# Optimization experiments

Hardware: AMD Instinct MI355X
Metric: run time of the kernel (lower is better)

Reference implementation:

```python
import jax, jax.numpy as jnp
import numpy as np

N, E, F, D = 50000, 800000, 128, 32
CUTOFF = 5.0


def swish(x):
    return x * jax.nn.sigmoid(x)


def setup_inputs() -> dict:
    key = jax.random.key(0)
    ks = jax.random.split(key, 15)
    sF = 1.0 / np.sqrt(F)
    inp = {
        "x": jax.random.normal(ks[0], (N, F), jnp.float32),
        # distances in [0, 6) so some edges lie beyond the 5.0 cutoff
        "rij": jax.random.uniform(ks[1], (E,), jnp.float32) * 6.0,
        "vij": jax.random.normal(ks[2], (E, 3), jnp.float32),
        "src": jax.random.randint(ks[3], (E,), 0, N),
        "dst": jax.random.randint(ks[4], (E,), 0, N),
        # transform: Dense(F,F,swish) -> Dense(F,D,swish)
        "W1": jax.random.normal(ks[5], (F, F), jnp.float32) * sF,
        "b1": jnp.zeros((F,), jnp.float32),
        "W2": jax.random.normal(ks[6], (F, D), jnp.float32) * sF,
        "b2": jnp.zeros((D,), jnp.float32),
        # transform2 (cross_product branch)
        "W1b": jax.random.normal(ks[7], (F, F), jnp.float32) * sF,
        "b1b": jnp.zeros((F,), jnp.float32),
        "W2b": jax.random.normal(ks[8], (F, D), jnp.float32) * sF,
        "b2b": jnp.zeros((D,), jnp.float32),
        # mix: Dense(3, 1), no activation
        "w_mix": jax.random.normal(ks[9], (3,), jnp.float32) * (1.0 / np.sqrt(3.0)),
        "b_mix": jnp.zeros((1,), jnp.float32),
    }
    return inp


def reference(x, rij, vij, src, dst, W1, b1, W2, b2, W1b, b1b, W2b, b2b, w_mix, b_mix):
    # node transforms: q, q2 in [N, D]
    q = swish(swish(x @ W1 + b1) @ W2 + b2)
    q2 = swish(swish(x @ W1b + b1b) @ W2b + b2b)

    # cosine cutoff on per-edge distance [E]
    c = 0.5 * (jnp.cos(jnp.pi * rij / CUTOFF) + 1.0)
    c = c * (rij < CUTOFF).astype(c.dtype)

    # e_mul_u: edge vij [E,1,3] * source-node q [E,D,1] -> [E,D,3], then cutoff scale
    mu_ij = vij[:, None, :] * q[src][:, :, None] * c[:, None, None]
    mu = jax.ops.segment_sum(mu_ij, dst, num_segments=N)  # [N,D,3]

    mu_ij2 = vij[:, None, :] * q2[src][:, :, None] * c[:, None, None]
    mu2 = jax.ops.segment_sum(mu_ij2, dst, num_segments=N)  # [N,D,3]

    mu3 = jnp.cross(mu, mu2, axis=-1)  # [N,D,3]
    stacked = jnp.stack([mu, mu2, mu3], axis=-1)  # [N,D,3,3]
    out = stacked @ w_mix + b_mix[0]  # mix Dense(3,1), squeezed -> [N,D,3]
    return out
```

## Files before the change

### kernel.cpp

```cpp
#include <hip/hip_runtime.h>
#include <hip/hip_bf16.h>

#define N_NODES 50000
#define E_EDGES 800000
#define F_DIM 128
#define D_DIM 32
#define CUTOFF 5.0f
#define PI_F 3.14159265358979f
#define SCAN_BLOCKS ((N_NODES + 255) / 256)

#define MLP_BLOCKS ((N_NODES + 31) / 32)
#define HIST_BLOCKS ((E_EDGES + 255) / 256)
#define XPAD 132

__device__ __forceinline__ float swishf(float x) { return x / (1.0f + expf(-x)); }

__global__ __launch_bounds__(256, 4)
void mlp_hist(const float* __restrict__ x,
              const float* __restrict__ W1a, const float* __restrict__ b1a,
              const float* __restrict__ W2a, const float* __restrict__ b2a,
              const float* __restrict__ W1b, const float* __restrict__ b1b,
              const float* __restrict__ W2b, const float* __restrict__ b2b,
              float* __restrict__ qq,
              const float* __restrict__ rij, const int* __restrict__ dst,
              int* __restrict__ deg) {
  if (blockIdx.x >= MLP_BLOCKS) {
    const int e = (blockIdx.x - MLP_BLOCKS) * 256 + threadIdx.x;
    if (e < E_EDGES && rij[e] < CUTOFF) atomicAdd(&deg[dst[e]], 1);
    return;
  }

  __shared__ float sX[64 * XPAD];

  const int rb = blockIdx.x * 32;
  const int t  = threadIdx.x;
  const int c  = t & 31;
  const int r0 = (t >> 5) * 4;

  {
    const int row = t >> 3;
    const int kq  = t & 7;
    const int rowG = min(rb + row, N_NODES - 1);
    const float* xp = x + (size_t)rowG * F_DIM;
#pragma unroll
    for (int p = 0; p < 4; ++p) {
      const int k0 = kq * 4 + p * 32;
      *(float4*)&sX[row * XPAD + k0] = *(const float4*)&xp[k0];
    }
  }
  __syncthreads();

  float accA[4][4], accB[4][4];
  {
    const float4 ba = *(const float4*)&b1a[4 * c];
    const float4 bb = *(const float4*)&b1b[4 * c];
#pragma unroll
    for (int r = 0; r < 4; ++r) {
      accA[r][0] = ba.x; accA[r][1] = ba.y; accA[r][2] = ba.z; accA[r][3] = ba.w;
      accB[r][0] = bb.x; accB[r][1] = bb.y; accB[r][2] = bb.z; accB[r][3] = bb.w;
    }
  }
  {
    const float* xrow = sX + r0 * XPAD;
    const float* wa_base = W1a + 4 * c;
    const float* wb_base = W1b + 4 * c;
#pragma unroll 2
    for (int k4 = 0; k4 < 32; ++k4) {
      float4 wa[4], wb[4];
#pragma unroll
      for (int kk = 0; kk < 4; ++kk) {
        const size_t off = (size_t)(k4 * 4 + kk) * F_DIM;
        wa[kk] = *(const float4*)(wa_base + off);
        wb[kk] = *(const float4*)(wb_base + off);
      }
      float4 xv[4];
#pragma unroll
      for (int r = 0; r < 4; ++r)
        xv[r] = *(const float4*)&xrow[r * XPAD + k4 * 4];
#pragma unroll
      for (int kk = 0; kk < 4; ++kk) {
#pragma unroll
        for (int r = 0; r < 4; ++r) {
          const float xs = (kk == 0) ? xv[r].x : (kk == 1) ? xv[r].y
                         : (kk == 2) ? xv[r].z : xv[r].w;
          accA[r][0] = fmaf(xs, wa[kk].x, accA[r][0]);
          accA[r][1] = fmaf(xs, wa[kk].y, accA[r][1]);
          accA[r][2] = fmaf(xs, wa[kk].z, accA[r][2]);
          accA[r][3] = fmaf(xs, wa[kk].w, accA[r][3]);
          accB[r][0] = fmaf(xs, wb[kk].x, accB[r][0]);
          accB[r][1] = fmaf(xs, wb[kk].y, accB[r][1]);
          accB[r][2] = fmaf(xs, wb[kk].z, accB[r][2]);
          accB[r][3] = fmaf(xs, wb[kk].w, accB[r][3]);
        }
      }
    }
  }

  __syncthreads();
#pragma unroll
  for (int r = 0; r < 4; ++r) {
    *(float4*)&sX[(r0 + r) * XPAD + 4 * c] =
        make_float4(swishf(accA[r][0]), swishf(accA[r][1]),
                    swishf(accA[r][2]), swishf(accA[r][3]));
    *(float4*)&sX[(32 + r0 + r) * XPAD + 4 * c] =
        make_float4(swishf(accB[r][0]), swishf(accB[r][1]),
                    swishf(accB[r][2]), swishf(accB[r][3]));
  }
  __syncthreads();

  float a2A[4], a2B[4];
  {
    const float bA = b2a[c];
    const float bB = b2b[c];
#pragma unroll
    for (int r = 0; r < 4; ++r) { a2A[r] = bA; a2B[r] = bB; }
  }
  {
    const float* hrowA = sX + r0 * XPAD;
    const float* hrowB = sX + (32 + r0) * XPAD;
#pragma unroll 2
    for (int k4 = 0; k4 < 32; ++k4) {
      float wA[4], wB[4];
#pragma unroll
      for (int kk = 0; kk < 4; ++kk) {
        wA[kk] = W2a[(size_t)(k4 * 4 + kk) * D_DIM + c];
        wB[kk] = W2b[(size_t)(k4 * 4 + kk) * D_DIM + c];
      }
      float4 hA[4], hB[4];
#pragma unroll
      for (int r = 0; r < 4; ++r) {
        hA[r] = *(const float4*)&hrowA[r * XPAD + k4 * 4];
        hB[r] = *(const float4*)&hrowB[r * XPAD + k4 * 4];
      }
#pragma unroll
      for (int kk = 0; kk < 4; ++kk) {
#pragma unroll
        for (int r = 0; r < 4; ++r) {
          const float hsA = (kk == 0) ? hA[r].x : (kk == 1) ? hA[r].y
                          : (kk == 2) ? hA[r].z : hA[r].w;
          const float hsB = (kk == 0) ? hB[r].x : (kk == 1) ? hB[r].y
                          : (kk == 2) ? hB[r].z : hB[r].w;
          a2A[r] = fmaf(hsA, wA[kk], a2A[r]);
          a2B[r] = fmaf(hsB, wB[kk], a2B[r]);
        }
      }
    }
  }

#pragma unroll
  for (int r = 0; r < 4; ++r) {
    const int row = rb + r0 + r;
    if (row < N_NODES) {
      *(float2*)&qq[(size_t)row * 64 + 2 * c] =
          make_float2(swishf(a2A[r]), swishf(a2B[r]));
    }
  }
}

__global__ __launch_bounds__(256)
void scan_blocksum(const int* __restrict__ deg, int* __restrict__ part) {
  __shared__ int red[256];
  const int t = threadIdx.x;
  const int i = blockIdx.x * 256 + t;
  red[t] = (i < N_NODES) ? deg[i] : 0;
  __syncthreads();
#pragma unroll
  for (int off = 128; off > 0; off >>= 1) {
    if (t < off) red[t] += red[t + off];
    __syncthreads();
  }
  if (t == 0) part[blockIdx.x] = red[0];
}

__global__ __launch_bounds__(256)
void scan_partials(int* __restrict__ part, int* __restrict__ row_start) {
  __shared__ int s[256];
  const int t = threadIdx.x;
  const int v = (t < SCAN_BLOCKS) ? part[t] : 0;
  s[t] = v;
  __syncthreads();
  for (int off = 1; off < 256; off <<= 1) {
    const int u = (t >= off) ? s[t - off] : 0;
    __syncthreads();
    s[t] += u;
    __syncthreads();
  }
  if (t < SCAN_BLOCKS) part[t] = s[t] - v;
  if (t == 255) row_start[N_NODES] = s[255];
}

__global__ __launch_bounds__(256)
void scan_write(const int* __restrict__ deg, const int* __restrict__ part,
                int* __restrict__ row_start, int* __restrict__ cursor) {
  __shared__ int s[256];
  const int t = threadIdx.x;
  const int i = blockIdx.x * 256 + t;
  const int v = (i < N_NODES) ? deg[i] : 0;
  s[t] = v;
  __syncthreads();
  for (int off = 1; off < 256; off <<= 1) {
    const int u = (t >= off) ? s[t - off] : 0;
    __syncthreads();
    s[t] += u;
    __syncthreads();
  }
  const int excl = s[t] - v + part[blockIdx.x];
  if (i < N_NODES) { row_start[i] = excl; cursor[i] = excl; }
}

__global__ __launch_bounds__(256)
void edge_reorder(const float* __restrict__ rij, const float* __restrict__ vij,
                  const int* __restrict__ src, const int* __restrict__ dst,
                  int* __restrict__ cursor, float4* __restrict__ recs) {
  const int e = blockIdx.x * 256 + threadIdx.x;
  if (e >= E_EDGES) return;
  const float r = rij[e];
  if (r >= CUTOFF) return;
  const float c = 0.5f * (cosf(r * (PI_F / CUTOFF)) + 1.0f);
  const int pos = atomicAdd(&cursor[dst[e]], 1);
  recs[pos] = make_float4(c * vij[3 * e + 0], c * vij[3 * e + 1],
                          c * vij[3 * e + 2], __int_as_float(src[e]));
}

__global__ __launch_bounds__(256)
void gather_out(const int* __restrict__ row_start, const float4* __restrict__ recs,
                const float2* __restrict__ qq,
                const float* __restrict__ w_mix, const float* __restrict__ b_mix,
                float* __restrict__ out) {
  const int tid = blockIdx.x * 256 + threadIdx.x;
  const int n = tid >> 5;
  const int d = tid & 31;
  if (n >= N_NODES) return;

  const int s0 = row_start[n];
  const int s1 = row_start[n + 1];

  float ax = 0.f, ay = 0.f, az = 0.f, bx = 0.f, by = 0.f, bz = 0.f;
  for (int i = s0; i < s1; i += 4) {
    const int i1 = min(i + 1, s1 - 1);
    const int i2 = min(i + 2, s1 - 1);
    const int i3 = min(i + 3, s1 - 1);
    float4 rc0 = recs[i];
    float4 rc1 = recs[i1];
    float4 rc2 = recs[i2];
    float4 rc3 = recs[i3];
    float2 p0 = qq[__float_as_int(rc0.w) * 32 + d];
    float2 p1 = qq[__float_as_int(rc1.w) * 32 + d];
    float2 p2 = qq[__float_as_int(rc2.w) * 32 + d];
    float2 p3 = qq[__float_as_int(rc3.w) * 32 + d];
    const float m1 = (i + 1 < s1) ? 1.f : 0.f;
    const float m2 = (i + 2 < s1) ? 1.f : 0.f;
    const float m3 = (i + 3 < s1) ? 1.f : 0.f;
    p1.x *= m1; p1.y *= m1;
    p2.x *= m2; p2.y *= m2;
    p3.x *= m3; p3.y *= m3;

    ax += rc0.x * p0.x + rc1.x * p1.x + rc2.x * p2.x + rc3.x * p3.x;
    ay += rc0.y * p0.x + rc1.y * p1.x + rc2.y * p2.x + rc3.y * p3.x;
    az += rc0.z * p0.x + rc1.z * p1.x + rc2.z * p2.x + rc3.z * p3.x;
    bx += rc0.x * p0.y + rc1.x * p1.y + rc2.x * p2.y + rc3.x * p3.y;
    by += rc0.y * p0.y + rc1.y * p1.y + rc2.y * p2.y + rc3.y * p3.y;
    bz += rc0.z * p0.y + rc1.z * p1.y + rc2.z * p2.y + rc3.z * p3.y;
  }

  const float cx = ay * bz - az * by;
  const float cy = az * bx - ax * bz;
  const float cz = ax * by - ay * bx;

  const float w0 = w_mix[0], w1 = w_mix[1], w2 = w_mix[2];
  const float bm = b_mix[0];

  const size_t base = (size_t)tid * 3;
  out[base + 0] = ax * w0 + bx * w1 + cx * w2 + bm;
  out[base + 1] = ay * w0 + by * w1 + cy * w2 + bm;
  out[base + 2] = az * w0 + bz * w1 + cz * w2 + bm;
}

extern "C" void kernel_launch(void* const* d_in, const int* in_sizes, int n_in,
                              void* d_out, int out_size, void* d_ws, size_t ws_size,
                              hipStream_t stream) {
  const float* x     = (const float*)d_in[0];
  const float* rij   = (const float*)d_in[1];
  const float* vij   = (const float*)d_in[2];
  const int*   src   = (const int*)  d_in[3];
  const int*   dst   = (const int*)  d_in[4];
  const float* W1    = (const float*)d_in[5];
  const float* b1    = (const float*)d_in[6];
  const float* W2    = (const float*)d_in[7];
  const float* b2    = (const float*)d_in[8];
  const float* W1b   = (const float*)d_in[9];
  const float* b1b   = (const float*)d_in[10];
  const float* W2b   = (const float*)d_in[11];
  const float* b2b   = (const float*)d_in[12];
  const float* w_mix = (const float*)d_in[13];
  const float* b_mix = (const float*)d_in[14];
  float* out = (float*)d_out;

  float4* recs   = (float4*)d_ws;
  float* qq      = (float*)(recs + E_EDGES);
  int* deg       = (int*)(qq + (size_t)N_NODES * 64);
  int* cursor    = deg + N_NODES;
  int* row_start = cursor + N_NODES;
  int* part      = row_start + N_NODES + 1;

  hipMemsetAsync(deg, 0, sizeof(int) * N_NODES, stream);

  mlp_hist<<<MLP_BLOCKS + HIST_BLOCKS, 256, 0, stream>>>(
      x, W1, b1, W2, b2, W1b, b1b, W2b, b2b, qq, rij, dst, deg);

  scan_blocksum<<<SCAN_BLOCKS, 256, 0, stream>>>(deg, part);
  scan_partials<<<1, 256, 0, stream>>>(part, row_start);
  scan_write<<<SCAN_BLOCKS, 256, 0, stream>>>(deg, part, row_start, cursor);

  const int eb = (E_EDGES + 255) / 256;
  edge_reorder<<<eb, 256, 0, stream>>>(rij, vij, src, dst, cursor, recs);

  gather_out<<<(N_NODES * D_DIM) / 256, 256, 0, stream>>>(
      row_start, recs, (const float2*)qq, w_mix, b_mix, out);
}
```

Measured before the change: 279.8 us.

## Split node MLP across histogram and reorder kernels to overlap edge passes

The node MLP blocks are split into two groups. The first 512 blocks run alongside the degree-histogram pass, and the remaining blocks are fused into the edge-reorder kernel. Edge blocks now come first in each grid, so the atomic-bound edge work overlaps with compute-bound MLP work in both launches. The MLP part is factored into a device function. The 512 split ratio is a tuning choice, and the edge kernel now carries the MLP's launch bounds and shared memory, which may reduce its occupancy.

```diff
diff --git a/kernel.cpp b/kernel.cpp
--- a/kernel.cpp
+++ b/kernel.cpp
@@ -10,29 +10,24 @@
 #define SCAN_BLOCKS ((N_NODES + 255) / 256)
 
 #define MLP_BLOCKS ((N_NODES + 31) / 32)
-#define HIST_BLOCKS ((E_EDGES + 255) / 256)
+#define MLP_PART1 512
+#define MLP_PART2 (MLP_BLOCKS - MLP_PART1)
+#define EDGE_BLOCKS ((E_EDGES + 255) / 256)
 #define XPAD 132
 
 __device__ __forceinline__ float swishf(float x) { return x / (1.0f + expf(-x)); }
 
-__global__ __launch_bounds__(256, 4)
-void mlp_hist(const float* __restrict__ x,
-              const float* __restrict__ W1a, const float* __restrict__ b1a,
-              const float* __restrict__ W2a, const float* __restrict__ b2a,
-              const float* __restrict__ W1b, const float* __restrict__ b1b,
-              const float* __restrict__ W2b, const float* __restrict__ b2b,
-              float* __restrict__ qq,
-              const float* __restrict__ rij, const int* __restrict__ dst,
-              int* __restrict__ deg) {
-  if (blockIdx.x >= MLP_BLOCKS) {
-    const int e = (blockIdx.x - MLP_BLOCKS) * 256 + threadIdx.x;
-    if (e < E_EDGES && rij[e] < CUTOFF) atomicAdd(&deg[dst[e]], 1);
-    return;
-  }
-
+__device__ __forceinline__ void mlp_body(
+    int mb,
+    const float* __restrict__ x,
+    const float* __restrict__ W1a, const float* __restrict__ b1a,
+    const float* __restrict__ W2a, const float* __restrict__ b2a,
+    const float* __restrict__ W1b, const float* __restrict__ b1b,
+    const float* __restrict__ W2b, const float* __restrict__ b2b,
+    float* __restrict__ qq) {
   __shared__ float sX[64 * XPAD];
 
-  const int rb = blockIdx.x * 32;
+  const int rb = mb * 32;
   const int t  = threadIdx.x;
   const int c  = t & 31;
   const int r0 = (t >> 5) * 4;
@@ -157,6 +152,48 @@
   }
 }
 
+__global__ __launch_bounds__(256, 4)
+void hist_mlp1(const float* __restrict__ x,
+               const float* __restrict__ W1a, const float* __restrict__ b1a,
+               const float* __restrict__ W2a, const float* __restrict__ b2a,
+               const float* __restrict__ W1b, const float* __restrict__ b1b,
+               const float* __restrict__ W2b, const float* __restrict__ b2b,
+               float* __restrict__ qq,
+               const float* __restrict__ rij, const int* __restrict__ dst,
+               int* __restrict__ deg) {
+  if (blockIdx.x < EDGE_BLOCKS) {
+    const int e = blockIdx.x * 256 + threadIdx.x;
+    if (e < E_EDGES && rij[e] < CUTOFF) atomicAdd(&deg[dst[e]], 1);
+    return;
+  }
+  mlp_body(blockIdx.x - EDGE_BLOCKS, x, W1a, b1a, W2a, b2a, W1b, b1b, W2b, b2b, qq);
+}
+
+__global__ __launch_bounds__(256, 4)
+void reorder_mlp2(const float* __restrict__ x,
+                  const float* __restrict__ W1a, const float* __restrict__ b1a,
+                  const float* __restrict__ W2a, const float* __restrict__ b2a,
+                  const float* __restrict__ W1b, const float* __restrict__ b1b,
+                  const float* __restrict__ W2b, const float* __restrict__ b2b,
+                  float* __restrict__ qq,
+                  const float* __restrict__ rij, const float* __restrict__ vij,
+                  const int* __restrict__ src, const int* __restrict__ dst,
+                  int* __restrict__ cursor, float4* __restrict__ recs) {
+  if (blockIdx.x < EDGE_BLOCKS) {
+    const int e = blockIdx.x * 256 + threadIdx.x;
+    if (e >= E_EDGES) return;
+    const float r = rij[e];
+    if (r >= CUTOFF) return;
+    const float c = 0.5f * (cosf(r * (PI_F / CUTOFF)) + 1.0f);
+    const int pos = atomicAdd(&cursor[dst[e]], 1);
+    recs[pos] = make_float4(c * vij[3 * e + 0], c * vij[3 * e + 1],
+                            c * vij[3 * e + 2], __int_as_float(src[e]));
+    return;
+  }
+  mlp_body(MLP_PART1 + (blockIdx.x - EDGE_BLOCKS),
+           x, W1a, b1a, W2a, b2a, W1b, b1b, W2b, b2b, qq);
+}
+
 __global__ __launch_bounds__(256)
 void scan_blocksum(const int* __restrict__ deg, int* __restrict__ part) {
   __shared__ int red[256];
@@ -206,20 +243,6 @@
   }
   const int excl = s[t] - v + part[blockIdx.x];
   if (i < N_NODES) { row_start[i] = excl; cursor[i] = excl; }
-}
-
-__global__ __launch_bounds__(256)
-void edge_reorder(const float* __restrict__ rij, const float* __restrict__ vij,
-                  const int* __restrict__ src, const int* __restrict__ dst,
-                  int* __restrict__ cursor, float4* __restrict__ recs) {
-  const int e = blockIdx.x * 256 + threadIdx.x;
-  if (e >= E_EDGES) return;
-  const float r = rij[e];
-  if (r >= CUTOFF) return;
-  const float c = 0.5f * (cosf(r * (PI_F / CUTOFF)) + 1.0f);
-  const int pos = atomicAdd(&cursor[dst[e]], 1);
-  recs[pos] = make_float4(c * vij[3 * e + 0], c * vij[3 * e + 1],
-                          c * vij[3 * e + 2], __int_as_float(src[e]));
 }
 
 __global__ __launch_bounds__(256)
@@ -305,15 +328,16 @@
 
   hipMemsetAsync(deg, 0, sizeof(int) * N_NODES, stream);
 
-  mlp_hist<<<MLP_BLOCKS + HIST_BLOCKS, 256, 0, stream>>>(
+  hist_mlp1<<<EDGE_BLOCKS + MLP_PART1, 256, 0, stream>>>(
       x, W1, b1, W2, b2, W1b, b1b, W2b, b2b, qq, rij, dst, deg);
 
   scan_blocksum<<<SCAN_BLOCKS, 256, 0, stream>>>(deg, part);
   scan_partials<<<1, 256, 0, stream>>>(part, row_start);
   scan_write<<<SCAN_BLOCKS, 256, 0, stream>>>(deg, part, row_start, cursor);
 
-  const int eb = (E_EDGES + 255) / 256;
-  edge_reorder<<<eb, 256, 0, stream>>>(rij, vij, src, dst, cursor, recs);
+  reorder_mlp2<<<EDGE_BLOCKS + MLP_PART2, 256, 0, stream>>>(
+      x, W1, b1, W2, b2, W1b, b1b, W2b, b2b, qq,
+      rij, vij, src, dst, cursor, recs);
 
   gather_out<<<(N_NODES * D_DIM) / 256, 256, 0, stream>>>(
       row_start, recs, (const float2*)qq, w_mix, b_mix, out);
```

Result: slower. 317.7 us (+13.5%).
